# Kernel tuning notes

Hardware: AMD Instinct MI355X
Metric: run time of the kernel (lower is better)

## Reference

```python
import jax, jax.numpy as jnp
import numpy as np

# ---- static config (mirrors init_kwargs) ----
NUM_ELEMENTS = 5
LATENT = 64            # latent_size / channel count C
SH_LMAX = 2            # spherical harmonics up to l=2
N_BASIS = 8            # n_radial_basis
MLP_HIDDEN = 64        # mlp_n_hidden (mlp_n_layers=2)
AVG_NUM_NEIGHBORS = 16.0
R_CUT = 5.0            # radial cutoff for bessel basis
N_GRAPHS = 100
NODES_PER_GRAPH = 200
N_NODES = N_GRAPHS * NODES_PER_GRAPH   # 20000
N_EDGES = 320000
NUM_RADII = 64         # len(jnp.arange(0.75, 2.03, 0.02))
POS_LMAX = 4
IRR_DIM = (POS_LMAX + 1) ** 2          # 25, dim of s2_irreps(4)
FLAT = LATENT * (1 + 3 + 5)            # flattened node-embedding dim = 576


def _sph(u):
    """Real spherical harmonics (component norm) of unit vectors u [E,3], l=1,2."""
    x, y, z = u[:, 0], u[:, 1], u[:, 2]
    sh1 = np.sqrt(3.0) * u  # [E,3]
    s15, s5 = np.sqrt(15.0), np.sqrt(5.0)
    sh2 = jnp.stack([
        s15 * x * y,
        s15 * y * z,
        0.5 * s5 * (3.0 * z * z - 1.0),
        s15 * x * z,
        0.5 * s15 * (x * x - y * y),
    ], axis=-1)  # [E,5]
    return sh1, sh2


def _radial_basis(r):
    """Bessel radial basis with smooth cosine cutoff. r: [E] -> [E, N_BASIS]."""
    n = jnp.arange(1, N_BASIS + 1, dtype=r.dtype)  # [B]
    rb = np.sqrt(2.0 / R_CUT) * jnp.sin(n[None, :] * jnp.pi * r[:, None] / R_CUT) / (r[:, None] + 1e-9)
    env = 0.5 * (jnp.cos(jnp.pi * jnp.minimum(r / R_CUT, 1.0)) + 1.0)
    return rb * env[:, None]


def setup_inputs() -> dict:
    key = jax.random.key(0)
    ks = jax.random.split(key, 24)
    C, H = LATENT, MLP_HIDDEN
    def w(k, shape, fan_in):
        return jax.random.normal(k, shape, dtype=jnp.float32) / np.sqrt(fan_in)
    return {
        "positions": jax.random.normal(ks[0], (N_NODES, 3), dtype=jnp.float32) * 3.0,
        "species": jax.random.randint(ks[1], (N_NODES,), 0, NUM_ELEMENTS),
        "senders": jax.random.randint(ks[2], (N_EDGES,), 0, N_NODES),
        "receivers": jax.random.randint(ks[3], (N_EDGES,), 0, N_NODES),
        "n_node": jnp.full((N_GRAPHS,), NODES_PER_GRAPH, dtype=jnp.int32),
        "target_species": jax.random.randint(ks[4], (N_GRAPHS,), 0, NUM_ELEMENTS),
        # learned parameters
        "species_embed": w(ks[5], (NUM_ELEMENTS, C), 1),
        "node_embed": w(ks[6], (NUM_ELEMENTS, C), 1),
        "radial_w1": w(ks[7], (N_BASIS, H), N_BASIS),
        "radial_w2": w(ks[8], (H, H), H),
        "radial_w3": w(ks[9], (H, C * (SH_LMAX + 1)), H),
        "lin_w0": w(ks[10], (C, C), C),
        "lin_w1": w(ks[11], (C, C), C),
        "lin_w2": w(ks[12], (C, C), C),
        "skip_w": w(ks[13], (NUM_ELEMENTS, C, C), C),
        "gate_w": w(ks[14], (C, 2 * C), C),
        "focus_w": w(ks[15], (FLAT, 1), FLAT),
        "focus_b": jnp.zeros((1,), dtype=jnp.float32),
        "species_w": w(ks[16], (FLAT, NUM_ELEMENTS), FLAT),
        "species_b": jnp.zeros((NUM_ELEMENTS,), dtype=jnp.float32),
        "pos_w": w(ks[17], (FLAT + C, NUM_RADII * IRR_DIM), FLAT + C),
        "pos_b": jnp.zeros((NUM_RADII * IRR_DIM,), dtype=jnp.float32),
    }


def reference(positions, species, senders, receivers, n_node, target_species,
              species_embed, node_embed, radial_w1, radial_w2, radial_w3,
              lin_w0, lin_w1, lin_w2, skip_w, gate_w,
              focus_w, focus_b, species_w, species_b, pos_w, pos_b):
    N = positions.shape[0]
    C = node_embed.shape[1]

    # --- node feature embedding (pure scalars 64x0e) ---
    h = node_embed[species]  # [N,C]

    # --- edge geometry: spherical harmonics + radial basis ---
    vec = positions[receivers] - positions[senders]          # [E,3]
    r = jnp.linalg.norm(vec, axis=-1)                        # [E]
    u = vec / (r[:, None] + 1e-9)
    sh1, sh2 = _sph(u)                                       # [E,3],[E,5]

    rb = _radial_basis(r)                                    # [E,B]
    hid = jax.nn.silu(rb @ radial_w1)
    hid = jax.nn.silu(hid @ radial_w2)
    wts = hid @ radial_w3                                    # [E, 3C]
    w0, w1, w2 = wts[:, :C], wts[:, C:2 * C], wts[:, 2 * C:] # per-l per-channel tp weights

    # --- CG tensor product messages (0e x Yl -> l, trivial CG for scalar inputs) ---
    hs = h[senders]                                          # [E,C]
    m0 = w0 * hs                                             # [E,C]   (l=0, Y0=1)
    m1 = (w1 * hs)[:, :, None] * sh1[:, None, :]             # [E,C,3]
    m2 = (w2 * hs)[:, :, None] * sh2[:, None, :]             # [E,C,5]

    # --- scatter-sum to receivers, normalized by sqrt(avg_num_neighbors) ---
    inv = 1.0 / np.sqrt(AVG_NUM_NEIGHBORS)
    a0 = jax.ops.segment_sum(m0, receivers, num_segments=N) * inv  # [N,C]
    a1 = jax.ops.segment_sum(m1, receivers, num_segments=N) * inv  # [N,C,3]
    a2 = jax.ops.segment_sum(m2, receivers, num_segments=N) * inv  # [N,C,5]

    # --- per-irrep linear to target_irreps + species-dependent self-interaction ---
    s = a0 @ lin_w0 + jnp.einsum('nc,ncd->nd', h, skip_w[species])  # [N,C]
    v = jnp.einsum('ncm,cd->ndm', a1, lin_w1)                       # [N,C,3]
    t = jnp.einsum('ncm,cd->ndm', a2, lin_w2)                       # [N,C,5]

    # --- gated nonlinearity: scalars via even activation, l>0 gated ---
    gates = jax.nn.sigmoid(s @ gate_w)                       # [N,2C]
    g1, g2 = gates[:, :C], gates[:, C:]
    s_out = jax.nn.silu(s)
    v_out = v * g1[:, :, None]
    t_out = t * g2[:, :, None]

    emb = jnp.concatenate([s_out, v_out.reshape(N, C * 3), t_out.reshape(N, C * 5)], axis=-1)  # [N,9C]

    # --- heads ---
    focus_logits = (emb @ focus_w + focus_b).squeeze(-1)     # [N]
    first_idx = jnp.concatenate([jnp.zeros((1,), n_node.dtype), jnp.cumsum(n_node)[:-1]])
    focus_emb = emb[first_idx]                               # [G,9C]
    tgt_emb = species_embed[target_species]                  # [G,C]
    species_logits = focus_emb @ species_w + species_b       # [G,5]
    pos_in = jnp.concatenate([focus_emb, tgt_emb], axis=-1)  # [G,9C+C]
    position_coeffs = (pos_in @ pos_w + pos_b).reshape(-1, NUM_RADII, IRR_DIM)  # [G,64,25]
    return focus_logits, species_logits, position_coeffs
```

## Files before the change

kernel.cpp:

```cpp
#include <hip/hip_runtime.h>
#include <hip/hip_bf16.h>
#include <math.h>

#define NNODES   20000
#define NEDGES   320000
#define NGRAPHS  100
#define CC       64
#define FLATDIM  576
#define POSIN    640
#define POSOUT   1600
#define PAYL     200
#define EPERM_N  320320

typedef __attribute__((ext_vector_type(8))) short bf16x8;
typedef __attribute__((ext_vector_type(4))) float f32x4;

__device__ __forceinline__ float silu_f(float x){ return x / (1.0f + __expf(-x)); }
__device__ __forceinline__ float sigm_f(float x){ return 1.0f / (1.0f + __expf(-x)); }
__device__ __forceinline__ unsigned pk_bf16(float lo, float hi){
    __hip_bfloat162 t;
    t.x = __float2bfloat16(lo);
    t.y = __float2bfloat16(hi);
    return *reinterpret_cast<unsigned*>(&t);
}
__device__ __forceinline__ unsigned short bf16u(float x){
    __hip_bfloat16 h = __float2bfloat16(x);
    return *reinterpret_cast<unsigned short*>(&h);
}
__device__ __forceinline__ float bf_lo(unsigned u){ return __uint_as_float(u << 16); }
__device__ __forceinline__ float bf_hi(unsigned u){ return __uint_as_float(u & 0xffff0000u); }
__device__ __forceinline__ float bfu(unsigned short u){ return __uint_as_float(((unsigned)u) << 16); }

__global__ void prep_kernel(const float* __restrict__ w1, const float* __restrict__ w2,
                            const float* __restrict__ w3,
                            const float* __restrict__ lw0, const float* __restrict__ lw1,
                            const float* __restrict__ lw2,
                            const float* __restrict__ skip_w, const float* __restrict__ node_embed,
                            const float* __restrict__ pos_w,
                            const int* __restrict__ n_node,
                            const int* __restrict__ senders,
                            const int* __restrict__ receivers,
                            const int* __restrict__ species,
                            unsigned* __restrict__ w1tn_g,
                            unsigned* __restrict__ w2tn_g, unsigned* __restrict__ w3l_g,
                            float* __restrict__ skip_vec,
                            unsigned* __restrict__ posw_bf,
                            int* __restrict__ flags, int* __restrict__ degree,
                            int* __restrict__ spcnt)
{
    __shared__ int cnt[5];
    if (threadIdx.x < 5) cnt[threadIdx.x] = 0;
    __syncthreads();

    int tid = blockIdx.x * blockDim.x + threadIdx.x;
    int stride = gridDim.x * blockDim.x;
    for (int i = tid; i < 256; i += stride) {
        int j = i >> 2, kp = (i & 3) * 2;
        w1tn_g[i] = pk_bf16(w1[kp * 64 + j], w1[(kp + 1) * 64 + j]);
    }
    for (int i = tid; i < 2048; i += stride) {
        int n = i >> 5, k = (i & 31) * 2;
        w2tn_g[i] = pk_bf16(w2[k * 64 + n], w2[(k + 1) * 64 + n]);
    }
    for (int i = tid; i < 15 * 2048; i += stride) {
        int sj = i >> 11;
        int sp = sj / 3, j = sj - sp * 3;
        int rem = i & 2047;
        int d = rem >> 5, kp = (rem & 31) * 2;
        const float* lw = (j == 0) ? lw0 : (j == 1) ? lw1 : lw2;
        float v0 = 0.f, v1 = 0.f;
        for (int c = 0; c < 64; c++) {
            float t = node_embed[sp * 64 + c] * lw[c * 64 + d];
            v0 += w3[kp * 192 + j * 64 + c] * t;
            v1 += w3[(kp + 1) * 192 + j * 64 + c] * t;
        }
        w3l_g[i] = pk_bf16(v0 * 0.25f, v1 * 0.25f);
    }
    for (int i = tid; i < 5 * 64; i += stride) {
        int sp = i >> 6, d = i & 63;
        float a = 0.0f;
        for (int c = 0; c < 64; c++)
            a += node_embed[sp * 64 + c] * skip_w[(sp * 64 + c) * 64 + d];
        skip_vec[i] = a;
    }
    for (int i = tid; i < 640 * 800; i += stride) {
        int k = i / 800, o = (i - k * 800) * 2;
        posw_bf[i] = pk_bf16(pos_w[(size_t)k * 1600 + o], pos_w[(size_t)k * 1600 + o + 1]);
    }
    for (int e = tid; e < NEDGES; e += stride) {
        atomicAdd(&degree[receivers[e]], 1);
        atomicAdd(&cnt[species[senders[e]]], 1);
    }
    if (tid == 0) {
        int a = 0;
        for (int g = 0; g < NGRAPHS; g++) { flags[a] = g + 1; a += n_node[g]; }
    }
    __syncthreads();
    if (threadIdx.x < 5 && cnt[threadIdx.x] > 0)
        atomicAdd(&spcnt[threadIdx.x], cnt[threadIdx.x]);
}

__global__ __launch_bounds__(1024) void scan_kernel(const int* __restrict__ degree,
                                                    const int* __restrict__ spcnt,
                                                    int* __restrict__ start,
                                                    int* __restrict__ pstart)
{
    __shared__ int partial[1024];
    int t = threadIdx.x;
    int base = t * 20;
    int s = 0;
    int loc[20];
    for (int i = 0; i < 20; i++) {
        int idx = base + i;
        int d = (idx < NNODES) ? degree[idx] : 0;
        loc[i] = s;
        s += d;
    }
    partial[t] = s;
    __syncthreads();
    if (t == 0) {
        int run = 0;
        for (int i = 0; i < 1024; i++) { int x = partial[i]; partial[i] = run; run += x; }
        start[NNODES] = run;
        int p = 0;
        for (int sp = 0; sp < 5; sp++) {
            pstart[sp] = p;
            p += ((spcnt[sp] + 63) >> 6) << 6;
        }
        pstart[5] = p;
    }
    __syncthreads();
    int off = partial[t];
    for (int i = 0; i < 20; i++) {
        int idx = base + i;
        if (idx < NNODES) start[idx] = off + loc[i];
    }
}

__global__ __launch_bounds__(256) void bucket_kernel(const int* __restrict__ senders,
                                                     const int* __restrict__ species,
                                                     const int* __restrict__ pstart,
                                                     int* __restrict__ grant,
                                                     int* __restrict__ eperm)
{
    __shared__ int cnt[5];
    __shared__ int base[5];
    int t = threadIdx.x;
    if (t < 5) cnt[t] = 0;
    __syncthreads();
    int e = blockIdx.x * 256 + t;
    int sp = species[senders[e]];
    int rank = atomicAdd(&cnt[sp], 1);
    __syncthreads();
    if (t < 5) base[t] = (cnt[t] > 0) ? atomicAdd(&grant[t], cnt[t]) : 0;
    __syncthreads();
    eperm[pstart[sp] + base[sp] + rank] = e;
}

__device__ __forceinline__ int swz(int row, int kbyte){
    return row * 128 + (kbyte ^ ((row & 7) << 4));
}
__device__ __forceinline__ bf16x8 ld_frag(const unsigned char* base, int row, int kbyte){
    return *reinterpret_cast<const bf16x8*>(base + swz(row, kbyte));
}
__device__ __forceinline__ bf16x8 ld_gfrag(const unsigned* base, int row, int kchunk){
    return *reinterpret_cast<const bf16x8*>(base + row * 32 + kchunk * 4);
}

__global__ __launch_bounds__(256, 4) void edge_kernel(
    const float* __restrict__ pos, const int* __restrict__ species,
    const int* __restrict__ senders, const int* __restrict__ receivers,
    const unsigned* __restrict__ w1tn_g,
    const unsigned* __restrict__ w2tn_g, const unsigned* __restrict__ w3l_g,
    const int* __restrict__ start, int* __restrict__ cursor,
    const int* __restrict__ eperm, const int* __restrict__ pstart,
    unsigned* __restrict__ payload)
{
    if (eperm[blockIdx.x * 64] < 0) return;

    __shared__ __align__(16) unsigned char a2l[8192];
    __shared__ __align__(16) unsigned short otl[64 * PAYL];
    __shared__ __align__(16) unsigned rblp[64 * 4];
    __shared__ int slotl[64];

    int tid = threadIdx.x;
    int w = tid >> 6, l = tid & 63;
    int lrow = l & 15;
    int kh = l >> 4;
    int lkb = kh * 16;

    int b64 = blockIdx.x * 64;
    int spb = 0;
    #pragma unroll
    for (int s = 1; s < 5; s++) if (b64 >= pstart[s]) spb = s;

    bf16x8 w2b0[4], w2b1[4];
    #pragma unroll
    for (int nt = 0; nt < 4; nt++) {
        w2b0[nt] = ld_gfrag(w2tn_g, nt * 16 + lrow, kh);
        w2b1[nt] = ld_gfrag(w2tn_g, nt * 16 + lrow, 4 + kh);
    }
    bf16x8 w3b0[3], w3b1[3];
    #pragma unroll
    for (int nl = 0; nl < 3; nl++) {
        int ntg = 3 * w + nl;
        int j  = ntg >> 2;
        int dt = ntg & 3;
        const unsigned* bb = w3l_g + (spb * 3 + j) * 2048;
        w3b0[nl] = ld_gfrag(bb, dt * 16 + lrow, kh);
        w3b1[nl] = ld_gfrag(bb, dt * 16 + lrow, 4 + kh);
    }
    bf16x8 w1b[4];
    #pragma unroll
    for (int nt = 0; nt < 4; nt++) {
        bf16x8 z = {0, 0, 0, 0, 0, 0, 0, 0};
        w1b[nt] = (kh == 0) ? *reinterpret_cast<const bf16x8*>(w1tn_g + (nt * 16 + lrow) * 4) : z;
    }

    if (tid < 64) {
        int e = eperm[b64 + tid];
        if (e >= 0) {
            int snd = senders[e];
            int rcv = receivers[e];
            slotl[tid] = start[rcv] + atomicAdd(&cursor[rcv], 1);

            float dx = pos[rcv * 3 + 0] - pos[snd * 3 + 0];
            float dy = pos[rcv * 3 + 1] - pos[snd * 3 + 1];
            float dz = pos[rcv * 3 + 2] - pos[snd * 3 + 2];
            float r = sqrtf(dx * dx + dy * dy + dz * dz);
            float rinv = 1.0f / (r + 1e-9f);
            float ux = dx * rinv, uy = dy * rinv, uz = dz * rinv;

            const float SQ3 = 1.7320508075688772f;
            const float S15 = 3.872983346207417f;
            const float S5  = 2.2360679774997896f;
            otl[tid * PAYL + 192] = bf16u(SQ3 * ux);
            otl[tid * PAYL + 193] = bf16u(SQ3 * uy);
            otl[tid * PAYL + 194] = bf16u(SQ3 * uz);
            otl[tid * PAYL + 195] = bf16u(S15 * ux * uy);
            otl[tid * PAYL + 196] = bf16u(S15 * uy * uz);
            otl[tid * PAYL + 197] = bf16u(0.5f * S5 * (3.0f * uz * uz - 1.0f));
            otl[tid * PAYL + 198] = bf16u(S15 * ux * uz);
            otl[tid * PAYL + 199] = bf16u(0.5f * S15 * (ux * ux - uy * uy));

            const float PI = 3.14159265358979323846f;
            float rc = r * 0.2f;
            float env = 0.5f * (__cosf(PI * fminf(rc, 1.0f)) + 1.0f);
            float scale = 0.6324555320336759f * rinv * env;
            float rb[8];
            #pragma unroll
            for (int b = 0; b < 8; b++) rb[b] = scale * __sinf((float)(b + 1) * PI * rc);
            #pragma unroll
            for (int p = 0; p < 4; p++)
                rblp[tid * 4 + p] = pk_bf16(rb[2 * p], rb[2 * p + 1]);
        } else {
            slotl[tid] = NEDGES;
            #pragma unroll
            for (int p = 0; p < 4; p++) rblp[tid * 4 + p] = 0;
            #pragma unroll
            for (int b = 0; b < 8; b++) otl[tid * PAYL + 192 + b] = 0;
        }
    }
    __syncthreads();

    {
        bf16x8 z = {0, 0, 0, 0, 0, 0, 0, 0};
        bf16x8 aRB = (kh == 0)
            ? *reinterpret_cast<const bf16x8*>(rblp + (16 * w + lrow) * 4) : z;
        #pragma unroll
        for (int nt = 0; nt < 4; nt++) {
            f32x4 c = {0.f, 0.f, 0.f, 0.f};
            c = __builtin_amdgcn_mfma_f32_16x16x32_bf16(aRB, w1b[nt], c, 0, 0, 0);
            int n = nt * 16 + lrow;
            #pragma unroll
            for (int r = 0; r < 4; r++) {
                int m = 16 * w + kh * 4 + r;
                *reinterpret_cast<unsigned short*>(a2l + swz(m, n * 2)) = bf16u(silu_f(c[r]));
            }
        }
    }
    __syncthreads();

    {
        bf16x8 aF0 = ld_frag(a2l, 16 * w + lrow, lkb);
        bf16x8 aF1 = ld_frag(a2l, 16 * w + lrow, 64 + lkb);
        f32x4 acc[4];
        #pragma unroll
        for (int nt = 0; nt < 4; nt++) {
            f32x4 c = {0.f, 0.f, 0.f, 0.f};
            c = __builtin_amdgcn_mfma_f32_16x16x32_bf16(aF0, w2b0[nt], c, 0, 0, 0);
            c = __builtin_amdgcn_mfma_f32_16x16x32_bf16(aF1, w2b1[nt], c, 0, 0, 0);
            acc[nt] = c;
        }
        __syncthreads();
        #pragma unroll
        for (int nt = 0; nt < 4; nt++) {
            int n = nt * 16 + lrow;
            #pragma unroll
            for (int r = 0; r < 4; r++) {
                int m = 16 * w + kh * 4 + r;
                *reinterpret_cast<unsigned short*>(a2l + swz(m, n * 2)) = bf16u(silu_f(acc[nt][r]));
            }
        }
    }
    __syncthreads();

    {
        #pragma unroll
        for (int mt = 0; mt < 4; mt++) {
            bf16x8 a30 = ld_frag(a2l, 16 * mt + lrow, lkb);
            bf16x8 a31 = ld_frag(a2l, 16 * mt + lrow, 64 + lkb);
            int mbase = 16 * mt + kh * 4;
            #pragma unroll
            for (int nl = 0; nl < 3; nl++) {
                f32x4 c = {0.f, 0.f, 0.f, 0.f};
                c = __builtin_amdgcn_mfma_f32_16x16x32_bf16(a30, w3b0[nl], c, 0, 0, 0);
                c = __builtin_amdgcn_mfma_f32_16x16x32_bf16(a31, w3b1[nl], c, 0, 0, 0);
                int o = (3 * w + nl) * 16 + lrow;
                otl[(mbase + 0) * PAYL + o] = bf16u(c[0]);
                otl[(mbase + 1) * PAYL + o] = bf16u(c[1]);
                otl[(mbase + 2) * PAYL + o] = bf16u(c[2]);
                otl[(mbase + 3) * PAYL + o] = bf16u(c[3]);
            }
        }
    }
    __syncthreads();

    {
        const uint4* ot4 = reinterpret_cast<const uint4*>(otl);
        uint4* pay4 = reinterpret_cast<uint4*>(payload);
        for (int i = tid; i < 64 * 25; i += 256) {
            int row = i / 25, q = i - row * 25;
            pay4[(size_t)slotl[row] * 25 + q] = ot4[row * 25 + q];
        }
    }
}

__global__ __launch_bounds__(256, 4) void node_kernel(
    const unsigned* __restrict__ payload, const int* __restrict__ start,
    const int* __restrict__ species, const float* __restrict__ skip_vec,
    const float* __restrict__ gate_w, const float* __restrict__ focus_w,
    const float* __restrict__ focus_b, const int* __restrict__ flags,
    const float* __restrict__ species_w, const float* __restrict__ species_b,
    float* __restrict__ out_focus, float* __restrict__ out_species,
    float* __restrict__ focus_emb)
{
    int wave = threadIdx.x >> 6;
    int lane = threadIdx.x & 63;
    int n = blockIdx.x * 4 + wave;

    __shared__ float ss[4][64];

    float a0 = 0, a1x = 0, a1y = 0, a1z = 0;
    float a2a = 0, a2b = 0, a2c = 0, a2d = 0, a2e = 0;
    float c0 = 0, c1x = 0, c1y = 0, c1z = 0;
    float c2a = 0, c2b = 0, c2c = 0, c2d = 0, c2e = 0;
    int s0 = start[n], s1 = start[n + 1];
    int i = s0;
    for (; i + 1 < s1; i += 2) {
        const unsigned short* pA = (const unsigned short*)(payload + (size_t)i * (PAYL / 2));
        const unsigned short* pB = (const unsigned short*)(payload + (size_t)(i + 1) * (PAYL / 2));
        float Ab0 = bfu(pA[lane]);
        float Ab1 = bfu(pA[64 + lane]);
        float Ab2 = bfu(pA[128 + lane]);
        uint4 Asv = *reinterpret_cast<const uint4*>(pA + 192);
        float Bb0 = bfu(pB[lane]);
        float Bb1 = bfu(pB[64 + lane]);
        float Bb2 = bfu(pB[128 + lane]);
        uint4 Bsv = *reinterpret_cast<const uint4*>(pB + 192);
        a0  += Ab0;
        a1x += Ab1 * bf_lo(Asv.x); a1y += Ab1 * bf_hi(Asv.x); a1z += Ab1 * bf_lo(Asv.y);
        a2a += Ab2 * bf_hi(Asv.y); a2b += Ab2 * bf_lo(Asv.z); a2c += Ab2 * bf_hi(Asv.z);
        a2d += Ab2 * bf_lo(Asv.w); a2e += Ab2 * bf_hi(Asv.w);
        c0  += Bb0;
        c1x += Bb1 * bf_lo(Bsv.x); c1y += Bb1 * bf_hi(Bsv.x); c1z += Bb1 * bf_lo(Bsv.y);
        c2a += Bb2 * bf_hi(Bsv.y); c2b += Bb2 * bf_lo(Bsv.z); c2c += Bb2 * bf_hi(Bsv.z);
        c2d += Bb2 * bf_lo(Bsv.w); c2e += Bb2 * bf_hi(Bsv.w);
    }
    if (i < s1) {
        const unsigned short* pA = (const unsigned short*)(payload + (size_t)i * (PAYL / 2));
        float Ab0 = bfu(pA[lane]);
        float Ab1 = bfu(pA[64 + lane]);
        float Ab2 = bfu(pA[128 + lane]);
        uint4 Asv = *reinterpret_cast<const uint4*>(pA + 192);
        a0  += Ab0;
        a1x += Ab1 * bf_lo(Asv.x); a1y += Ab1 * bf_hi(Asv.x); a1z += Ab1 * bf_lo(Asv.y);
        a2a += Ab2 * bf_hi(Asv.y); a2b += Ab2 * bf_lo(Asv.z); a2c += Ab2 * bf_hi(Asv.z);
        a2d += Ab2 * bf_lo(Asv.w); a2e += Ab2 * bf_hi(Asv.w);
    }
    float s  = a0 + c0 + skip_vec[species[n] * 64 + lane];
    float v0 = a1x + c1x, v1 = a1y + c1y, v2 = a1z + c1z;
    float t0 = a2a + c2a, t1 = a2b + c2b, t2 = a2c + c2c, t3 = a2d + c2d, t4 = a2e + c2e;

    ss[wave][lane] = s;
    float g1a = 0.0f, g2a = 0.0f;
    #pragma unroll 4
    for (int c = 0; c < 64; c++) {
        float sc = ss[wave][c];
        g1a += sc * gate_w[c * 128 + lane];
        g2a += sc * gate_w[c * 128 + 64 + lane];
    }
    float g1 = sigm_f(g1a), g2 = sigm_f(g2a);
    float s_out = s * sigm_f(s);
    float vo0 = v0 * g1, vo1 = v1 * g1, vo2 = v2 * g1;
    float to0 = t0 * g2, to1 = t1 * g2, to2 = t2 * g2, to3 = t3 * g2, to4 = t4 * g2;

    float pfo = s_out * focus_w[lane]
              + vo0 * focus_w[64 + lane * 3 + 0]
              + vo1 * focus_w[64 + lane * 3 + 1]
              + vo2 * focus_w[64 + lane * 3 + 2]
              + to0 * focus_w[256 + lane * 5 + 0]
              + to1 * focus_w[256 + lane * 5 + 1]
              + to2 * focus_w[256 + lane * 5 + 2]
              + to3 * focus_w[256 + lane * 5 + 3]
              + to4 * focus_w[256 + lane * 5 + 4];
    #pragma unroll
    for (int off = 32; off > 0; off >>= 1) pfo += __shfl_down(pfo, off);
    if (lane == 0) out_focus[n] = pfo + focus_b[0];

    int fg = flags[n];
    if (fg) {
        float* fe = focus_emb + (size_t)(fg - 1) * FLATDIM;
        fe[lane] = s_out;
        fe[64 + lane * 3 + 0] = vo0;
        fe[64 + lane * 3 + 1] = vo1;
        fe[64 + lane * 3 + 2] = vo2;
        fe[256 + lane * 5 + 0] = to0;
        fe[256 + lane * 5 + 1] = to1;
        fe[256 + lane * 5 + 2] = to2;
        fe[256 + lane * 5 + 3] = to3;
        fe[256 + lane * 5 + 4] = to4;

        #pragma unroll
        for (int j = 0; j < 5; j++) {
            float acc = s_out * species_w[lane * 5 + j]
                      + vo0 * species_w[(64 + lane * 3 + 0) * 5 + j]
                      + vo1 * species_w[(64 + lane * 3 + 1) * 5 + j]
                      + vo2 * species_w[(64 + lane * 3 + 2) * 5 + j]
                      + to0 * species_w[(256 + lane * 5 + 0) * 5 + j]
                      + to1 * species_w[(256 + lane * 5 + 1) * 5 + j]
                      + to2 * species_w[(256 + lane * 5 + 2) * 5 + j]
                      + to3 * species_w[(256 + lane * 5 + 3) * 5 + j]
                      + to4 * species_w[(256 + lane * 5 + 4) * 5 + j];
            #pragma unroll
            for (int off = 32; off > 0; off >>= 1) acc += __shfl_down(acc, off);
            if (lane == 0) out_species[(fg - 1) * 5 + j] = acc + species_b[j];
        }
    }
}

__global__ __launch_bounds__(256) void pos_kernel(
    const float* __restrict__ focus_emb, const int* __restrict__ target_species,
    const float* __restrict__ species_embed,
    const unsigned* __restrict__ posw_bf,
    float* __restrict__ partial)
{
    int g  = blockIdx.x >> 4;
    int ks = blockIdx.x & 15;
    int k0 = ks * 40;
    int tid = threadIdx.x;
    __shared__ float pin[40];

    if (tid < 40) {
        int k = k0 + tid;
        pin[tid] = (k < FLATDIM) ? focus_emb[(size_t)g * FLATDIM + k]
                                 : species_embed[target_species[g] * CC + (k - FLATDIM)];
    }
    __syncthreads();

    if (tid < 200) {
        float a0 = 0, a1 = 0, a2 = 0, a3 = 0, a4 = 0, a5 = 0, a6 = 0, a7 = 0;
        const unsigned* wp = posw_bf + (size_t)k0 * 800 + tid * 4;
        #pragma unroll 4
        for (int kk = 0; kk < 40; kk++) {
            uint4 wv = *reinterpret_cast<const uint4*>(wp + (size_t)kk * 800);
            float p = pin[kk];
            a0 += p * bf_lo(wv.x); a1 += p * bf_hi(wv.x);
            a2 += p * bf_lo(wv.y); a3 += p * bf_hi(wv.y);
            a4 += p * bf_lo(wv.z); a5 += p * bf_hi(wv.z);
            a6 += p * bf_lo(wv.w); a7 += p * bf_hi(wv.w);
        }
        float* op = partial + ((size_t)(g * 16 + ks)) * POSOUT + tid * 8;
        *reinterpret_cast<float4*>(op)     = make_float4(a0, a1, a2, a3);
        *reinterpret_cast<float4*>(op + 4) = make_float4(a4, a5, a6, a7);
    }
}

__global__ __launch_bounds__(256) void posred_kernel(
    const float* __restrict__ partial, const float* __restrict__ pos_b,
    float* __restrict__ out_pos)
{
    int g    = blockIdx.x >> 1;
    int half = blockIdx.x & 1;
    const float* pg = partial + (size_t)g * 16 * POSOUT;
    for (int o = half * 800 + threadIdx.x; o < half * 800 + 800; o += 256) {
        float a = pos_b[o];
        #pragma unroll
        for (int ks = 0; ks < 16; ks++) a += pg[ks * POSOUT + o];
        out_pos[(size_t)g * POSOUT + o] = a;
    }
}

extern "C" void kernel_launch(void* const* d_in, const int* in_sizes, int n_in,
                              void* d_out, int out_size, void* d_ws, size_t ws_size,
                              hipStream_t stream) {
    const float* positions      = (const float*)d_in[0];
    const int*   species        = (const int*)  d_in[1];
    const int*   senders        = (const int*)  d_in[2];
    const int*   receivers      = (const int*)  d_in[3];
    const int*   n_node         = (const int*)  d_in[4];
    const int*   target_species = (const int*)  d_in[5];
    const float* species_embed  = (const float*)d_in[6];
    const float* node_embed     = (const float*)d_in[7];
    const float* radial_w1      = (const float*)d_in[8];
    const float* radial_w2      = (const float*)d_in[9];
    const float* radial_w3      = (const float*)d_in[10];
    const float* lin_w0         = (const float*)d_in[11];
    const float* lin_w1         = (const float*)d_in[12];
    const float* lin_w2         = (const float*)d_in[13];
    const float* skip_w         = (const float*)d_in[14];
    const float* gate_w         = (const float*)d_in[15];
    const float* focus_w        = (const float*)d_in[16];
    const float* focus_b        = (const float*)d_in[17];
    const float* species_w      = (const float*)d_in[18];
    const float* species_b      = (const float*)d_in[19];
    const float* pos_w          = (const float*)d_in[20];
    const float* pos_b          = (const float*)d_in[21];

    unsigned* payload = (unsigned*)d_ws;
    float*    partial = (float*)d_ws;
    unsigned* posw_bf = payload + (size_t)(NEDGES + 4) * (PAYL / 2);
    int* eperm  = (int*)(posw_bf + 640 * 800);
    int* degree = eperm + EPERM_N;
    int* cursor = degree + NNODES;
    int* flags  = cursor + NNODES;
    int* spcnt  = flags + NNODES;
    int* grant  = spcnt + 5;
    int* start  = grant + 5 + 6;
    int* pstart = start + NNODES + 1;
    unsigned* w1tn_g = (unsigned*)(pstart + 6);
    unsigned* w2tn_g = w1tn_g + 256;
    unsigned* w3l_g  = w2tn_g + 2048;
    float* skip_vec  = (float*)(w3l_g + 15 * 2048);
    float* focus_emb = skip_vec + 320;

    float* out       = (float*)d_out;
    float* out_focus = out;
    float* out_spec  = out + NNODES;
    float* out_pos   = out + NNODES + NGRAPHS * 5;

    hipMemsetAsync(eperm, 0xFF, EPERM_N * sizeof(int), stream);
    hipMemsetAsync(degree, 0, (3 * NNODES + 16) * sizeof(int), stream);

    prep_kernel<<<512, 256, 0, stream>>>(radial_w1, radial_w2, radial_w3,
                                         lin_w0, lin_w1, lin_w2,
                                         skip_w, node_embed, pos_w, n_node,
                                         senders, receivers, species,
                                         w1tn_g, w2tn_g, w3l_g, skip_vec, posw_bf,
                                         flags, degree, spcnt);
    scan_kernel<<<1, 1024, 0, stream>>>(degree, spcnt, start, pstart);
    bucket_kernel<<<NEDGES / 256, 256, 0, stream>>>(senders, species, pstart, grant, eperm);

    edge_kernel<<<EPERM_N / 64, 256, 0, stream>>>(
        positions, species, senders, receivers,
        w1tn_g, w2tn_g, w3l_g, start, cursor, eperm, pstart, payload);

    node_kernel<<<NNODES / 4, 256, 0, stream>>>(
        payload, start, species, skip_vec,
        gate_w, focus_w, focus_b, flags,
        species_w, species_b, out_focus, out_spec, focus_emb);

    pos_kernel<<<NGRAPHS * 16, 256, 0, stream>>>(
        focus_emb, target_species, species_embed, posw_bf, partial);

    posred_kernel<<<NGRAPHS * 2, 256, 0, stream>>>(partial, pos_b, out_pos);
}
```

Before: 195.5 us.

## Halve edge-kernel output staging LDS and raise occupancy; move flag setup into scan

The edge kernel's output staging buffer shrinks from 64 rows to 32 rows. The MFMA output tiles are now written and flushed to global memory in two halves, and the spherical-harmonic values go into a small separate LDS array. Together with launch bounds raised from 4 to 6 blocks per SM, this is meant to cut LDS use so more blocks can be resident. It costs an extra barrier pair per half. The serial graph-flag loop on a single thread moves from prep_kernel into scan_kernel, where each of 100 threads computes its own offset.

Result: slower. 207.4 us (+6.1%).

```diff
diff --git a/kernel.cpp b/kernel.cpp
--- a/kernel.cpp
+++ b/kernel.cpp
@@ -37,7 +37,6 @@
                             const float* __restrict__ lw2,
                             const float* __restrict__ skip_w, const float* __restrict__ node_embed,
                             const float* __restrict__ pos_w,
-                            const int* __restrict__ n_node,
                             const int* __restrict__ senders,
                             const int* __restrict__ receivers,
                             const int* __restrict__ species,
@@ -45,7 +44,7 @@
                             unsigned* __restrict__ w2tn_g, unsigned* __restrict__ w3l_g,
                             float* __restrict__ skip_vec,
                             unsigned* __restrict__ posw_bf,
-                            int* __restrict__ flags, int* __restrict__ degree,
+                            int* __restrict__ degree,
                             int* __restrict__ spcnt)
 {
     __shared__ int cnt[5];
@@ -91,10 +90,6 @@
         atomicAdd(&degree[receivers[e]], 1);
         atomicAdd(&cnt[species[senders[e]]], 1);
     }
-    if (tid == 0) {
-        int a = 0;
-        for (int g = 0; g < NGRAPHS; g++) { flags[a] = g + 1; a += n_node[g]; }
-    }
     __syncthreads();
     if (threadIdx.x < 5 && cnt[threadIdx.x] > 0)
         atomicAdd(&spcnt[threadIdx.x], cnt[threadIdx.x]);
@@ -102,11 +97,20 @@
 
 __global__ __launch_bounds__(1024) void scan_kernel(const int* __restrict__ degree,
                                                     const int* __restrict__ spcnt,
+                                                    const int* __restrict__ n_node,
                                                     int* __restrict__ start,
-                                                    int* __restrict__ pstart)
+                                                    int* __restrict__ pstart,
+                                                    int* __restrict__ flags)
 {
     __shared__ int partial[1024];
     int t = threadIdx.x;
+
+    if (t < NGRAPHS) {
+        int off = 0;
+        for (int g = 0; g < t; g++) off += n_node[g];
+        flags[off] = t + 1;
+    }
+
     int base = t * 20;
     int s = 0;
     int loc[20];
@@ -167,7 +171,7 @@
     return *reinterpret_cast<const bf16x8*>(base + row * 32 + kchunk * 4);
 }
 
-__global__ __launch_bounds__(256, 4) void edge_kernel(
+__global__ __launch_bounds__(256, 6) void edge_kernel(
     const float* __restrict__ pos, const int* __restrict__ species,
     const int* __restrict__ senders, const int* __restrict__ receivers,
     const unsigned* __restrict__ w1tn_g,
@@ -179,7 +183,8 @@
     if (eperm[blockIdx.x * 64] < 0) return;
 
     __shared__ __align__(16) unsigned char a2l[8192];
-    __shared__ __align__(16) unsigned short otl[64 * PAYL];
+    __shared__ __align__(16) unsigned short otl[32 * 192];
+    __shared__ __align__(16) unsigned short shl[64 * 8];
     __shared__ __align__(16) unsigned rblp[64 * 4];
     __shared__ int slotl[64];
 
@@ -234,14 +239,14 @@
             const float SQ3 = 1.7320508075688772f;
             const float S15 = 3.872983346207417f;
             const float S5  = 2.2360679774997896f;
-            otl[tid * PAYL + 192] = bf16u(SQ3 * ux);
-            otl[tid * PAYL + 193] = bf16u(SQ3 * uy);
-            otl[tid * PAYL + 194] = bf16u(SQ3 * uz);
-            otl[tid * PAYL + 195] = bf16u(S15 * ux * uy);
-            otl[tid * PAYL + 196] = bf16u(S15 * uy * uz);
-            otl[tid * PAYL + 197] = bf16u(0.5f * S5 * (3.0f * uz * uz - 1.0f));
-            otl[tid * PAYL + 198] = bf16u(S15 * ux * uz);
-            otl[tid * PAYL + 199] = bf16u(0.5f * S15 * (ux * ux - uy * uy));
+            shl[tid * 8 + 0] = bf16u(SQ3 * ux);
+            shl[tid * 8 + 1] = bf16u(SQ3 * uy);
+            shl[tid * 8 + 2] = bf16u(SQ3 * uz);
+            shl[tid * 8 + 3] = bf16u(S15 * ux * uy);
+            shl[tid * 8 + 4] = bf16u(S15 * uy * uz);
+            shl[tid * 8 + 5] = bf16u(0.5f * S5 * (3.0f * uz * uz - 1.0f));
+            shl[tid * 8 + 6] = bf16u(S15 * ux * uz);
+            shl[tid * 8 + 7] = bf16u(0.5f * S15 * (ux * ux - uy * uy));
 
             const float PI = 3.14159265358979323846f;
             float rc = r * 0.2f;
@@ -258,7 +263,7 @@
             #pragma unroll
             for (int p = 0; p < 4; p++) rblp[tid * 4 + p] = 0;
             #pragma unroll
-            for (int b = 0; b < 8; b++) otl[tid * PAYL + 192 + b] = 0;
+            for (int b = 0; b < 8; b++) shl[tid * 8 + b] = 0;
         }
     }
     __syncthreads();
@@ -305,34 +310,45 @@
     }
     __syncthreads();
 
-    {
+    const uint4* sh4 = reinterpret_cast<const uint4*>(shl);
+    uint4* pay4 = reinterpret_cast<uint4*>(payload);
+    #pragma unroll
+    for (int mhalf = 0; mhalf < 2; mhalf++) {
         #pragma unroll
-        for (int mt = 0; mt < 4; mt++) {
+        for (int mtl = 0; mtl < 2; mtl++) {
+            int mt = mhalf * 2 + mtl;
             bf16x8 a30 = ld_frag(a2l, 16 * mt + lrow, lkb);
             bf16x8 a31 = ld_frag(a2l, 16 * mt + lrow, 64 + lkb);
-            int mbase = 16 * mt + kh * 4;
+            int mbase = 16 * mtl + kh * 4;
             #pragma unroll
             for (int nl = 0; nl < 3; nl++) {
                 f32x4 c = {0.f, 0.f, 0.f, 0.f};
                 c = __builtin_amdgcn_mfma_f32_16x16x32_bf16(a30, w3b0[nl], c, 0, 0, 0);
                 c = __builtin_amdgcn_mfma_f32_16x16x32_bf16(a31, w3b1[nl], c, 0, 0, 0);
                 int o = (3 * w + nl) * 16 + lrow;
-                otl[(mbase + 0) * PAYL + o] = bf16u(c[0]);
-                otl[(mbase + 1) * PAYL + o] = bf16u(c[1]);
-                otl[(mbase + 2) * PAYL + o] = bf16u(c[2]);
-                otl[(mbase + 3) * PAYL + o] = bf16u(c[3]);
+                otl[(mbase + 0) * 192 + o] = bf16u(c[0]);
+                otl[(mbase + 1) * 192 + o] = bf16u(c[1]);
+                otl[(mbase + 2) * 192 + o] = bf16u(c[2]);
+                otl[(mbase + 3) * 192 + o] = bf16u(c[3]);
             }
         }
-    }
-    __syncthreads();
-
-    {
-        const uint4* ot4 = reinterpret_cast<const uint4*>(otl);
-        uint4* pay4 = reinterpret_cast<uint4*>(payload);
-        for (int i = tid; i < 64 * 25; i += 256) {
-            int row = i / 25, q = i - row * 25;
-            pay4[(size_t)slotl[row] * 25 + q] = ot4[row * 25 + q];
-        }
+        __syncthreads();
+
+        {
+            const uint4* ot4 = reinterpret_cast<const uint4*>(otl);
+            int row = tid >> 3;
+            int grow = mhalf * 32 + row;
+            size_t basep = (size_t)slotl[grow] * 25;
+            int baser = row * 24;
+            int q0 = tid & 7;
+            #pragma unroll
+            for (int j = 0; j < 4; j++) {
+                int q = q0 + 8 * j;
+                if (q < 24) pay4[basep + q] = ot4[baser + q];
+                else if (q == 24) pay4[basep + 24] = sh4[grow];
+            }
+        }
+        __syncthreads();
     }
 }
 
@@ -554,11 +570,11 @@
 
     prep_kernel<<<512, 256, 0, stream>>>(radial_w1, radial_w2, radial_w3,
                                          lin_w0, lin_w1, lin_w2,
-                                         skip_w, node_embed, pos_w, n_node,
+                                         skip_w, node_embed, pos_w,
                                          senders, receivers, species,
                                          w1tn_g, w2tn_g, w3l_g, skip_vec, posw_bf,
-                                         flags, degree, spcnt);
-    scan_kernel<<<1, 1024, 0, stream>>>(degree, spcnt, start, pstart);
+                                         degree, spcnt);
+    scan_kernel<<<1, 1024, 0, stream>>>(degree, spcnt, n_node, start, pstart, flags);
     bucket_kernel<<<NEDGES / 256, 256, 0, stream>>>(senders, species, pstart, grant, eperm);
 
     edge_kernel<<<EPERM_N / 64, 256, 0, stream>>>(
```
